# Performance work log

Hardware: AMD Instinct MI355X
Metric: run time of the kernel (lower is better)

Reference implementation:

```python
import jax, jax.numpy as jnp
import numpy as np

BATCH = 4
N = 50000   # mesh nodes
LAT = 10    # latent dim n
K = 32      # neighbours per node
M = [64, 64, 256]  # hotness MLP dims; M[-1] = number of clusters
MU = 1.0
B0 = 2.0


def _linear_params(key, out_dim, in_dim):
    kw, _ = jax.random.split(key)
    w = jax.random.normal(kw, (out_dim, in_dim), jnp.float32) * np.sqrt(2.0 / in_dim)
    b = jnp.zeros((out_dim,), jnp.float32)
    return w, b


def setup_inputs() -> dict:
    key = jax.random.key(0)
    ks = jax.random.split(key, 12)
    x = jax.random.normal(ks[0], (BATCH, N), jnp.float32)
    neighbour_id = jax.random.randint(ks[1], (N, K), 0, N)
    # small distances so bubble windows have nonzero support everywhere
    neighbour_distance = jax.random.uniform(ks[2], (N, K), jnp.float32) * 0.05
    clustering_labels = jax.random.randint(ks[3], (N,), 0, M[-1])
    enc1_w, enc1_b = _linear_params(ks[4], 200, N)
    enc2_w, enc2_b = _linear_params(ks[5], LAT, 200)
    dec_w, dec_b = _linear_params(ks[6], N, LAT)
    h1_w, h1_b = _linear_params(ks[7], M[0], LAT)
    h2_w, h2_b = _linear_params(ks[8], M[1], M[0])
    h3_w, h3_b = _linear_params(ks[9], M[2], M[1])
    B_param = jnp.array(B0, jnp.float32)
    return dict(x=x, neighbour_id=neighbour_id, neighbour_distance=neighbour_distance,
                clustering_labels=clustering_labels,
                enc1_w=enc1_w, enc1_b=enc1_b, enc2_w=enc2_w, enc2_b=enc2_b,
                dec_w=dec_w, dec_b=dec_b,
                h1_w=h1_w, h1_b=h1_b, h2_w=h2_w, h2_b=h2_b, h3_w=h3_w, h3_b=h3_b,
                B_param=B_param)


def _silu(v):
    return v * jax.nn.sigmoid(v)


def reference(x, neighbour_id, neighbour_distance, clustering_labels,
              enc1_w, enc1_b, enc2_w, enc2_b, dec_w, dec_b,
              h1_w, h1_b, h2_w, h2_b, h3_w, h3_b, B_param):
    # encode: [b, N] -> [b, n]
    z = _silu(x @ enc1_w.T + enc1_b)
    e = z @ enc2_w.T + enc2_b  # [b, n]

    # hotness MLP on latent codes (batched over b): silu on all but last layer
    h = _silu(e @ h1_w.T + h1_b)
    h = _silu(h @ h2_w.T + h2_b)
    h = h @ h3_w.T + h3_b
    h = jax.nn.sigmoid(h * 0.005)  # [b, n_clusters]

    # per-node hotness via cluster labels -> per-sample, per-basis bandwidths
    H = h[:, clustering_labels]  # [b, N]
    exps = jnp.arange(1, LAT + 1, dtype=jnp.float32)  # [n]
    w = (1.0 - H / 2.0)[:, None, :] ** exps[None, :, None] * B_param  # [b, n, N]

    # RBF bubble window over neighbours, normalized over k
    d2 = neighbour_distance ** 2  # [N, k]
    win = jnp.maximum(0.0, 1.0 - d2[None, None, :, :] / (w * MU)[..., None] ** 2)  # [b,n,N,k]
    win = win / jnp.sum(win, axis=-1, keepdims=True)

    # gather decoder basis rows at neighbours: dec_w.T is [n, N]
    basis = dec_w.T[:, neighbour_id]  # [n, N, k]
    conv = jnp.einsum('nNk,bnNk->bnN', basis, win)  # convolved basis [b, n, N]

    out = jnp.einsum('bn,bnN->bN', e, conv) + dec_b  # [b, N]
    return out
```

## Files before the change

### kernel.cpp

```cpp
#include <hip/hip_runtime.h>
#include <math.h>

#define NN        50000
#define BATCH     4
#define LAT       10
#define KNB       32
#define E1OUT     200
#define NCHUNK    8
#define CHUNK2    3125

__device__ __forceinline__ float silu_f(float v) {
    return v / (1.0f + expf(-v));
}

__global__ __launch_bounds__(256) void k0_pad(const float* __restrict__ dec_w,
                                              float* __restrict__ dec_pad) {
    const int i = blockIdx.x * 256 + threadIdx.x;
    if (i >= NN * 16) return;
    const int r = i >> 4, c = i & 15;
    dec_pad[i] = (c < LAT) ? dec_w[r * LAT + c] : 0.0f;
}

__global__ __launch_bounds__(256) void k1_partial(const float* __restrict__ x,
                                                  const float* __restrict__ w,
                                                  float* __restrict__ partials) {
    const int bx  = blockIdx.x;
    const int r   = bx >> 3;
    const int c   = bx & 7;
    const int tid = threadIdx.x;

    const float2* wr = (const float2*)w + (size_t)r * 25000 + c * CHUNK2;
    const float2* x0 = (const float2*)x + 0 * 25000 + c * CHUNK2;
    const float2* x1 = (const float2*)x + 1 * 25000 + c * CHUNK2;
    const float2* x2 = (const float2*)x + 2 * 25000 + c * CHUNK2;
    const float2* x3 = (const float2*)x + 3 * 25000 + c * CHUNK2;

    float a0 = 0.f, a1 = 0.f, a2 = 0.f, a3 = 0.f;
    for (int j = tid; j < CHUNK2; j += 256) {
        float2 wv = wr[j];
        float2 v0 = x0[j], v1 = x1[j], v2 = x2[j], v3 = x3[j];
        a0 = fmaf(wv.x, v0.x, fmaf(wv.y, v0.y, a0));
        a1 = fmaf(wv.x, v1.x, fmaf(wv.y, v1.y, a1));
        a2 = fmaf(wv.x, v2.x, fmaf(wv.y, v2.y, a2));
        a3 = fmaf(wv.x, v3.x, fmaf(wv.y, v3.y, a3));
    }

    __shared__ float sm[4][256];
    sm[0][tid] = a0; sm[1][tid] = a1; sm[2][tid] = a2; sm[3][tid] = a3;
    __syncthreads();
    for (int s = 128; s > 0; s >>= 1) {
        if (tid < s) {
            sm[0][tid] += sm[0][tid + s];
            sm[1][tid] += sm[1][tid + s];
            sm[2][tid] += sm[2][tid + s];
            sm[3][tid] += sm[3][tid + s];
        }
        __syncthreads();
    }
    if (tid < 4) partials[bx * 4 + tid] = sm[tid][0];
}

__global__ __launch_bounds__(256) void k2_small(
        const float* __restrict__ partials,
        const float* __restrict__ enc1_b,
        const float* __restrict__ enc2_w, const float* __restrict__ enc2_b,
        const float* __restrict__ h1_w,   const float* __restrict__ h1_b,
        const float* __restrict__ h2_w,   const float* __restrict__ h2_b,
        const float* __restrict__ h3_w,   const float* __restrict__ h3_b,
        float* __restrict__ ws_e, float* __restrict__ ws_h) {
    __shared__ float zs[BATCH][E1OUT];
    __shared__ float es[BATCH][LAT];
    __shared__ float h1s[BATCH][64];
    __shared__ float h2s[BATCH][64];
    const int t = threadIdx.x;

    if (t < E1OUT) {
        float a0 = 0.f, a1 = 0.f, a2 = 0.f, a3 = 0.f;
        for (int cc = 0; cc < NCHUNK; ++cc) {
            const float* p = partials + (t * NCHUNK + cc) * 4;
            a0 += p[0]; a1 += p[1]; a2 += p[2]; a3 += p[3];
        }
        float bias = enc1_b[t];
        zs[0][t] = silu_f(a0 + bias);
        zs[1][t] = silu_f(a1 + bias);
        zs[2][t] = silu_f(a2 + bias);
        zs[3][t] = silu_f(a3 + bias);
    }
    __syncthreads();

    if (t < BATCH * LAT) {
        int b = t / LAT, l = t % LAT;
        const float* wrow = enc2_w + l * E1OUT;
        float a = 0.f;
        for (int o = 0; o < E1OUT; ++o) a = fmaf(zs[b][o], wrow[o], a);
        a += enc2_b[l];
        es[b][l] = a;
        ws_e[b * LAT + l] = a;
    }
    __syncthreads();

    {
        int b = t >> 6, u = t & 63;
        float a = h1_b[u];
        const float* wrow = h1_w + u * LAT;
        #pragma unroll
        for (int l = 0; l < LAT; ++l) a = fmaf(es[b][l], wrow[l], a);
        h1s[b][u] = silu_f(a);
    }
    __syncthreads();

    {
        int b = t >> 6, u = t & 63;
        float a = h2_b[u];
        const float* wrow = h2_w + u * 64;
        for (int j = 0; j < 64; ++j) a = fmaf(h1s[b][j], wrow[j], a);
        h2s[b][u] = silu_f(a);
    }
    __syncthreads();

    {
        const float* wrow = h3_w + t * 64;
        float bias = h3_b[t];
        #pragma unroll
        for (int b = 0; b < BATCH; ++b) {
            float a = bias;
            for (int j = 0; j < 64; ++j) a = fmaf(h2s[b][j], wrow[j], a);
            ws_h[b * 256 + t] = 1.0f / (1.0f + expf(-0.005f * a));
        }
    }
}

__global__ __launch_bounds__(256) void k3_main(
        const int*   __restrict__ nid,
        const float* __restrict__ nd,
        const int*   __restrict__ labels,
        const float* __restrict__ dec_pad,
        const float* __restrict__ dec_b,
        const float* __restrict__ Bp,
        const float* __restrict__ ws_e,
        const float* __restrict__ ws_h,
        float* __restrict__ out) {
    __shared__ float hs[BATCH * 256];
    __shared__ float es[BATCH * LAT];
    const int tid = threadIdx.x;
    for (int i = tid; i < BATCH * 256; i += 256) hs[i] = ws_h[i];
    if (tid < BATCH * LAT) es[tid] = ws_e[tid];
    __syncthreads();

    const int gid = blockIdx.x * 256 + tid;
    const int n   = gid >> 3;
    if (n >= NN) return;
    const int b   = tid & 3;
    const int kh  = (tid >> 2) & 1;

    const float Bv = Bp[0];
    const int   c  = labels[n];

    float invw2[LAT];
    {
        const float H    = hs[b * 256 + c];
        const float base = 1.0f - 0.5f * H;
        float cur = base;
        #pragma unroll
        for (int l = 0; l < LAT; ++l) {
            const float wv = cur * Bv;
            invw2[l] = 1.0f / (wv * wv);
            cur *= base;
        }
    }

    float num[LAT], den[LAT];
    #pragma unroll
    for (int l = 0; l < LAT; ++l) { num[l] = 0.f; den[l] = 0.f; }

    const int4*   nid4 = (const int4*)nid + (size_t)n * 8 + kh * 4;
    const float4* nd4  = (const float4*)nd  + (size_t)n * 8 + kh * 4;

    #pragma unroll
    for (int kk = 0; kk < 4; ++kk) {
        const int4   id4 = nid4[kk];
        const float4 dd4 = nd4[kk];
        const int   ids[4] = {id4.x, id4.y, id4.z, id4.w};
        const float dsv[4] = {dd4.x, dd4.y, dd4.z, dd4.w};
        #pragma unroll
        for (int q = 0; q < 4; ++q) {
            const float d2 = dsv[q] * dsv[q];
            const float* row = dec_pad + (size_t)ids[q] * 16;
            const float4 r0 = *(const float4*)(row);
            const float4 r1 = *(const float4*)(row + 4);
            const float2 r2 = *(const float2*)(row + 8);
            const float bas[LAT] = {r0.x, r0.y, r0.z, r0.w,
                                    r1.x, r1.y, r1.z, r1.w,
                                    r2.x, r2.y};
            #pragma unroll
            for (int l = 0; l < LAT; ++l) {
                float t = fmaf(-d2, invw2[l], 1.0f);
                t = fmaxf(t, 0.0f);
                den[l] += t;
                num[l]  = fmaf(t, bas[l], num[l]);
            }
        }
    }

    #pragma unroll
    for (int l = 0; l < LAT; ++l) {
        num[l] += __shfl_xor(num[l], 4);
        den[l] += __shfl_xor(den[l], 4);
    }

    if (kh == 0) {
        float acc = 0.f;
        #pragma unroll
        for (int l = 0; l < LAT; ++l)
            acc = fmaf(es[b * LAT + l], num[l] / den[l], acc);
        out[(size_t)b * NN + n] = acc + dec_b[n];
    }
}

extern "C" void kernel_launch(void* const* d_in, const int* in_sizes, int n_in,
                              void* d_out, int out_size, void* d_ws, size_t ws_size,
                              hipStream_t stream) {
    const float* x      = (const float*)d_in[0];
    const int*   nid    = (const int*)  d_in[1];
    const float* nd     = (const float*)d_in[2];
    const int*   labels = (const int*)  d_in[3];
    const float* enc1_w = (const float*)d_in[4];
    const float* enc1_b = (const float*)d_in[5];
    const float* enc2_w = (const float*)d_in[6];
    const float* enc2_b = (const float*)d_in[7];
    const float* dec_w  = (const float*)d_in[8];
    const float* dec_b  = (const float*)d_in[9];
    const float* h1_w   = (const float*)d_in[10];
    const float* h1_b   = (const float*)d_in[11];
    const float* h2_w   = (const float*)d_in[12];
    const float* h2_b   = (const float*)d_in[13];
    const float* h3_w   = (const float*)d_in[14];
    const float* h3_b   = (const float*)d_in[15];
    const float* Bp     = (const float*)d_in[16];

    float* ws       = (float*)d_ws;
    float* partials = ws;
    float* ws_e     = ws + 6400;
    float* ws_h     = ws + 6440;
    float* dec_pad  = ws + 8192;
    float* out      = (float*)d_out;

    k0_pad<<<(NN * 16 + 255) / 256, 256, 0, stream>>>(dec_w, dec_pad);
    k1_partial<<<E1OUT * NCHUNK, 256, 0, stream>>>(x, enc1_w, partials);
    k2_small<<<1, 256, 0, stream>>>(partials, enc1_b, enc2_w, enc2_b,
                                    h1_w, h1_b, h2_w, h2_b, h3_w, h3_b,
                                    ws_e, ws_h);
    const int k3_threads = NN * 8;
    k3_main<<<(k3_threads + 255) / 256, 256, 0, stream>>>(
        nid, nd, labels, dec_pad, dec_b, Bp, ws_e, ws_h, out);
}
```

Baseline: 179.1 us.

## Merge pad kernel into encoder GEMM launch and split neighbours four ways

```diff
diff --git a/kernel.cpp b/kernel.cpp
--- a/kernel.cpp
+++ b/kernel.cpp
@@ -8,26 +8,33 @@
 #define E1OUT     200
 #define NCHUNK    8
 #define CHUNK2    3125
+#define K1BLOCKS  (E1OUT * NCHUNK)
+#define PADBLOCKS ((NN * 16 + 255) / 256)
 
 __device__ __forceinline__ float silu_f(float v) {
     return v / (1.0f + expf(-v));
 }
 
-__global__ __launch_bounds__(256) void k0_pad(const float* __restrict__ dec_w,
-                                              float* __restrict__ dec_pad) {
-    const int i = blockIdx.x * 256 + threadIdx.x;
-    if (i >= NN * 16) return;
-    const int r = i >> 4, c = i & 15;
-    dec_pad[i] = (c < LAT) ? dec_w[r * LAT + c] : 0.0f;
-}
-
-__global__ __launch_bounds__(256) void k1_partial(const float* __restrict__ x,
-                                                  const float* __restrict__ w,
-                                                  float* __restrict__ partials) {
+__global__ __launch_bounds__(256) void kA_gemm_pad(
+        const float* __restrict__ x,
+        const float* __restrict__ w,
+        const float* __restrict__ dec_w,
+        float* __restrict__ partials,
+        float* __restrict__ dec_pad) {
     const int bx  = blockIdx.x;
-    const int r   = bx >> 3;
-    const int c   = bx & 7;
     const int tid = threadIdx.x;
+
+    if (bx >= K1BLOCKS) {
+        const int i = (bx - K1BLOCKS) * 256 + tid;
+        if (i < NN * 16) {
+            const int r = i >> 4, c = i & 15;
+            dec_pad[i] = (c < LAT) ? dec_w[r * LAT + c] : 0.0f;
+        }
+        return;
+    }
+
+    const int r = bx >> 3;
+    const int c = bx & 7;
 
     const float2* wr = (const float2*)w + (size_t)r * 25000 + c * CHUNK2;
     const float2* x0 = (const float2*)x + 0 * 25000 + c * CHUNK2;
@@ -148,10 +155,10 @@
     __syncthreads();
 
     const int gid = blockIdx.x * 256 + tid;
-    const int n   = gid >> 3;
+    const int n   = gid >> 4;
     if (n >= NN) return;
     const int b   = tid & 3;
-    const int kh  = (tid >> 2) & 1;
+    const int kq  = (tid >> 2) & 3;
 
     const float Bv = Bp[0];
     const int   c  = labels[n];
@@ -173,11 +180,11 @@
     #pragma unroll
     for (int l = 0; l < LAT; ++l) { num[l] = 0.f; den[l] = 0.f; }
 
-    const int4*   nid4 = (const int4*)nid + (size_t)n * 8 + kh * 4;
-    const float4* nd4  = (const float4*)nd  + (size_t)n * 8 + kh * 4;
+    const int4*   nid4 = (const int4*)nid + (size_t)n * 8 + kq * 2;
+    const float4* nd4  = (const float4*)nd  + (size_t)n * 8 + kq * 2;
 
     #pragma unroll
-    for (int kk = 0; kk < 4; ++kk) {
+    for (int kk = 0; kk < 2; ++kk) {
         const int4   id4 = nid4[kk];
         const float4 dd4 = nd4[kk];
         const int   ids[4] = {id4.x, id4.y, id4.z, id4.w};
@@ -206,9 +213,11 @@
     for (int l = 0; l < LAT; ++l) {
         num[l] += __shfl_xor(num[l], 4);
         den[l] += __shfl_xor(den[l], 4);
-    }
-
-    if (kh == 0) {
+        num[l] += __shfl_xor(num[l], 8);
+        den[l] += __shfl_xor(den[l], 8);
+    }
+
+    if (kq == 0) {
         float acc = 0.f;
         #pragma unroll
         for (int l = 0; l < LAT; ++l)
@@ -245,12 +254,11 @@
     float* dec_pad  = ws + 8192;
     float* out      = (float*)d_out;
 
-    k0_pad<<<(NN * 16 + 255) / 256, 256, 0, stream>>>(dec_w, dec_pad);
-    k1_partial<<<E1OUT * NCHUNK, 256, 0, stream>>>(x, enc1_w, partials);
+    kA_gemm_pad<<<K1BLOCKS + PADBLOCKS, 256, 0, stream>>>(
+        x, enc1_w, dec_w, partials, dec_pad);
     k2_small<<<1, 256, 0, stream>>>(partials, enc1_b, enc2_w, enc2_b,
                                     h1_w, h1_b, h2_w, h2_b, h3_w, h3_b,
                                     ws_e, ws_h);
-    const int k3_threads = NN * 8;
-    k3_main<<<(k3_threads + 255) / 256, 256, 0, stream>>>(
+    k3_main<<<(NN * 16 + 255) / 256, 256, 0, stream>>>(
         nid, nd, labels, dec_pad, dec_b, Bp, ws_e, ws_h, out);
 }
```

Measured after the change: 175.6 us. No clear change (-2.0%).
